# Kernel optimization log

Measured on AMD Instinct MI355X. Metric: run time of the kernel, lower is better.

Reference implementation:

```python
import jax, jax.numpy as jnp
import numpy as np

B, S, E, H, DK = 16, 512, 256, 8, 32
NSH, NSEL = 2, 4           # shared heads, selected dynamic heads
NDYN = H - NSH             # dynamic heads
NB = 4                     # num_blocks -> blocks_1: NB layers, blocks_2: 2*NB layers
L = 3 * NB                 # total layers, params stacked on leading dim
NSKILL, NQ = 1000, 10000
FC1, FC2 = 512, 256


def setup_inputs():
    key = jax.random.key(0)
    ks = jax.random.split(key, 24)
    r = lambda i, sh: jax.random.normal(ks[i], sh, jnp.float32) * 0.02
    return {
        'skills': jax.random.randint(ks[0], (B, S), 0, NSKILL),
        'responses': jax.random.randint(ks[1], (B, S), 0, 2),
        'questions': jax.random.randint(ks[2], (B, S), 0, NQ),
        'attention_mask': jnp.ones((B, S), jnp.int32),
        'q_embed': r(3, (NSKILL, E)),
        'qa_embed': r(4, (3, E)),
        'q_embed_diff': r(5, (NSKILL + 1, E)),
        'qa_embed_diff': r(6, (2 * NSKILL + 1, E)),
        'difficult_param': r(7, (NQ + 1, 1)),
        'Wq': r(8, (L, E, E)), 'bq': jnp.zeros((L, E)),
        'Wv': r(9, (L, E, E)), 'bv': jnp.zeros((L, E)),
        'Wo': r(10, (L, E, E)), 'bo': jnp.zeros((L, E)),
        'Wg': r(11, (L, E, NDYN)),
        'ln1_g': jnp.ones((L, E)), 'ln1_b': jnp.zeros((L, E)),
        'ln2_g': jnp.ones((L, E)), 'ln2_b': jnp.zeros((L, E)),
        'ffn_W1': r(12, (L, E, E)), 'ffn_b1': jnp.zeros((L, E)),
        'ffn_W2': r(13, (L, E, E)), 'ffn_b2': jnp.zeros((L, E)),
        'out_W1': r(14, (2 * E, FC1)), 'out_b1': jnp.zeros((FC1,)),
        'out_W2': r(15, (FC1, FC2)), 'out_b2': jnp.zeros((FC2,)),
        'out_W3': r(16, (FC2, 1)), 'out_b3': jnp.zeros((1,)),
    }


def _ln(x, g, b):
    m = x.mean(-1, keepdims=True)
    v = ((x - m) ** 2).mean(-1, keepdims=True)
    return (x - m) * jax.lax.rsqrt(v + 1e-5) * g + b


def _layer(i, q_in, k_in, v_in, mask, P):
    # MoH attention: standard MHA + top-k routed dynamic heads (kq_same=True)
    qh = (q_in @ P['Wq'][i] + P['bq'][i]).reshape(B, S, H, DK).transpose(0, 2, 1, 3)
    kh = (k_in @ P['Wq'][i] + P['bq'][i]).reshape(B, S, H, DK).transpose(0, 2, 1, 3)
    vh = (v_in @ P['Wv'][i] + P['bv'][i]).reshape(B, S, H, DK).transpose(0, 2, 1, 3)
    scores = jnp.einsum('bhid,bhjd->bhij', qh, kh) / np.float32(np.sqrt(DK))
    attn = jax.nn.softmax(jnp.where(mask, scores, -1e32), axis=-1)
    ctx = jnp.einsum('bhij,bhjd->bhid', attn, vh).transpose(0, 2, 1, 3)  # [B,S,H,DK]
    # router on pre-projection query: hard top-NSEL one-hot gates over NDYN heads
    logits = q_in @ P['Wg'][i]                     # [B,S,NDYN]
    _, topi = jax.lax.top_k(logits, NSEL)
    gates = jax.nn.one_hot(topi, NDYN, dtype=ctx.dtype).sum(-2)
    hg = jnp.concatenate([jnp.ones((B, S, NSH), ctx.dtype), gates], axis=-1)  # [B,S,H]
    attn_out = (ctx * hg[..., None]).reshape(B, S, E) @ P['Wo'][i] + P['bo'][i]
    x = _ln(q_in + attn_out, P['ln1_g'][i], P['ln1_b'][i])
    f = jax.nn.relu(x @ P['ffn_W1'][i] + P['ffn_b1'][i]) @ P['ffn_W2'][i] + P['ffn_b2'][i]
    return _ln(x + f, P['ln2_g'][i], P['ln2_b'][i])


def _forward(skills, responses, questions, P):
    masked_r = responses * (responses > -1).astype(responses.dtype)
    q_emb = P['q_embed'][skills]
    qa_emb = q_emb + P['qa_embed'][masked_r]
    q_diff = P['q_embed_diff'][skills]
    pid = P['difficult_param'][questions]          # [B,S,1]
    q_emb = q_emb + pid * q_diff
    qa_diff = P['qa_embed_diff'][skills + NSKILL * masked_r]
    qa_emb = qa_emb + pid * (qa_diff + q_diff)
    idx = jnp.arange(S)
    causal = (idx[None, :] <= idx[:, None])[None, None]  # mask==1: incl diagonal
    strict = (idx[None, :] < idx[:, None])[None, None]   # mask==0: excl diagonal
    y, x = qa_emb, q_emb
    for i in range(NB):
        y = _layer(i, y, y, y, causal, P)
    li = NB
    for _ in range(NB):
        x = _layer(li, x, x, x, causal, P); li += 1
        x = _layer(li, x, x, y, strict, P); li += 1
    h = jnp.concatenate([x, q_emb], axis=-1)
    h = jax.nn.relu(h @ P['out_W1'] + P['out_b1'])
    h = jax.nn.relu(h @ P['out_W2'] + P['out_b2'])
    out = jax.nn.sigmoid(h @ P['out_W3'] + P['out_b3'])[..., 0]
    return out[:, 1:]


def reference(skills, responses, questions, attention_mask, q_embed, qa_embed, q_embed_diff, qa_embed_diff, difficult_param, Wq, bq, Wv, bv, Wo, bo, Wg, ln1_g, ln1_b, ln2_g, ln2_b, ffn_W1, ffn_b1, ffn_W2, ffn_b2, out_W1, out_b1, out_W2, out_b2, out_W3, out_b3):
    P = dict(q_embed=q_embed, qa_embed=qa_embed, q_embed_diff=q_embed_diff, qa_embed_diff=qa_embed_diff, difficult_param=difficult_param, Wq=Wq, bq=bq, Wv=Wv, bv=bv, Wo=Wo, bo=bo, Wg=Wg, ln1_g=ln1_g, ln1_b=ln1_b, ln2_g=ln2_g, ln2_b=ln2_b, ffn_W1=ffn_W1, ffn_b1=ffn_b1, ffn_W2=ffn_W2, ffn_b2=ffn_b2, out_W1=out_W1, out_b1=out_b1, out_W2=out_W2, out_b2=out_b2, out_W3=out_W3, out_b3=out_b3)
    return _forward(skills, responses, questions, P)
```

## Files before the change

kernel.cpp:

```cpp
#include <hip/hip_runtime.h>
#include <hip/hip_bf16.h>

constexpr int CB = 16, CS = 512, CE = 256, CH = 8, CDK = 32;
constexpr int CNDYN = 6;
constexpr int CT = CB * CS;
constexpr float SCALE = 0.17677669529663687f;

typedef __bf16 bf16x8 __attribute__((ext_vector_type(8)));
typedef float f32x4 __attribute__((ext_vector_type(4)));
typedef unsigned short u16x8 __attribute__((ext_vector_type(8)));

__device__ __forceinline__ unsigned short f2bf(float x) {
    union { float f; unsigned u; } v; v.f = x;
    unsigned r = v.u + 0x7fff + ((v.u >> 16) & 1);
    return (unsigned short)(r >> 16);
}

__global__ __launch_bounds__(256) void embed_kernel(
    const int* __restrict__ skills, const int* __restrict__ responses,
    const int* __restrict__ questions,
    const float* __restrict__ q_embed, const float* __restrict__ qa_embed,
    const float* __restrict__ q_embed_diff, const float* __restrict__ qa_embed_diff,
    const float* __restrict__ difficult,
    float* __restrict__ q_emb, float* __restrict__ qa_emb, float* __restrict__ xb)
{
    int t = blockIdx.x;
    int e = threadIdx.x;
    int sk = skills[t];
    int r  = responses[t];
    r = (r > -1) ? r : 0;
    float pid = difficult[questions[t]];
    float qe  = q_embed[(size_t)sk * CE + e];
    float qd  = q_embed_diff[(size_t)sk * CE + e];
    float qv  = qe + pid * qd;
    float qae = qe + qa_embed[(size_t)r * CE + e];
    float qad = qa_embed_diff[((size_t)sk + 1000 * r) * CE + e];
    float qav = qae + pid * (qad + qd);
    q_emb[(size_t)t * CE + e]  = qv;
    xb[(size_t)t * CE + e]     = qv;
    qa_emb[(size_t)t * CE + e] = qav;
}

__device__ __forceinline__ void transpose_tile(
    const float* __restrict__ src, unsigned short* __restrict__ dst, int K, int N)
{
    __shared__ unsigned short T[64][72];
    int k0 = blockIdx.y * 64, n0 = blockIdx.x * 64;
    int t = threadIdx.x;
    int kr = t >> 3, nsg = (t & 7) * 8;
#pragma unroll
    for (int rr = 0; rr < 64; rr += 32) {
        const float* p = src + (size_t)(k0 + kr + rr) * N + n0 + nsg;
        float4 a = *reinterpret_cast<const float4*>(p);
        float4 b = *reinterpret_cast<const float4*>(p + 4);
        int k = kr + rr;
        T[nsg + 0][k] = f2bf(a.x); T[nsg + 1][k] = f2bf(a.y);
        T[nsg + 2][k] = f2bf(a.z); T[nsg + 3][k] = f2bf(a.w);
        T[nsg + 4][k] = f2bf(b.x); T[nsg + 5][k] = f2bf(b.y);
        T[nsg + 6][k] = f2bf(b.z); T[nsg + 7][k] = f2bf(b.w);
    }
    __syncthreads();
    {
        int n = t >> 2, ks = (t & 3) * 16;
        unsigned short* dp = dst + (size_t)(n0 + n) * K + k0 + ks;
        *reinterpret_cast<u16x8*>(dp)     = *reinterpret_cast<const u16x8*>(&T[n][ks]);
        *reinterpret_cast<u16x8*>(dp + 8) = *reinterpret_cast<const u16x8*>(&T[n][ks + 8]);
    }
}

__global__ __launch_bounds__(256) void prep_w_layers(
    const float* __restrict__ Wq, const float* __restrict__ Wv,
    const float* __restrict__ Wo, const float* __restrict__ W1,
    const float* __restrict__ W2,
    unsigned short* __restrict__ qvT, unsigned short* __restrict__ woT,
    unsigned short* __restrict__ w1T, unsigned short* __restrict__ w2T)
{
    int z = blockIdx.z;
    int which = z / 12, l = z % 12;
    const float* src;
    unsigned short* dst;
    if      (which == 0) { src = Wq + (size_t)l * 65536; dst = qvT + (size_t)l * 131072; }
    else if (which == 1) { src = Wv + (size_t)l * 65536; dst = qvT + (size_t)l * 131072 + 65536; }
    else if (which == 2) { src = Wo + (size_t)l * 65536; dst = woT + (size_t)l * 65536; }
    else if (which == 3) { src = W1 + (size_t)l * 65536; dst = w1T + (size_t)l * 65536; }
    else                 { src = W2 + (size_t)l * 65536; dst = w2T + (size_t)l * 65536; }
    transpose_tile(src, dst, 256, 256);
}

__global__ __launch_bounds__(256) void prep_w_one(
    const float* __restrict__ src, unsigned short* __restrict__ dst, int K, int N)
{
    transpose_tile(src, dst, K, N);
}

__global__ __launch_bounds__(256) void gemm_mfma(
    const float* __restrict__ A, const unsigned short* __restrict__ WT,
    const float* __restrict__ bias, float* __restrict__ C,
    const float* __restrict__ bias2, float* __restrict__ C2,
    const unsigned char* __restrict__ gmask,
    int M, int N, int K, int relu, int split)
{
    __shared__ __attribute__((aligned(16))) unsigned short As[64][72];
    __shared__ __attribute__((aligned(16))) unsigned short Bs[64][72];
    int tid = threadIdx.x;
    int bm = blockIdx.y * 64, bn = blockIdx.x * 64;
    int w = tid >> 6, lane = tid & 63;
    int wr = w >> 1, wc = w & 1;
    int lo = lane & 15, hi = lane >> 4;
    int srow = tid >> 2, sseg = (tid & 3) * 16;
    f32x4 acc[2][2] = {};

    for (int kk = 0; kk < K; kk += 64) {
        {
            const float* ap = A + (size_t)(bm + srow) * K + kk + sseg;
            float4 a0 = *reinterpret_cast<const float4*>(ap);
            float4 a1 = *reinterpret_cast<const float4*>(ap + 4);
            float4 a2 = *reinterpret_cast<const float4*>(ap + 8);
            float4 a3 = *reinterpret_cast<const float4*>(ap + 12);
            if (gmask) {
                int hh = (kk + sseg) >> 5;
                float km = ((gmask[bm + srow] >> hh) & 1) ? 1.f : 0.f;
                a0.x*=km; a0.y*=km; a0.z*=km; a0.w*=km;
                a1.x*=km; a1.y*=km; a1.z*=km; a1.w*=km;
                a2.x*=km; a2.y*=km; a2.z*=km; a2.w*=km;
                a3.x*=km; a3.y*=km; a3.z*=km; a3.w*=km;
            }
            u16x8 p0, p1;
            p0[0]=f2bf(a0.x); p0[1]=f2bf(a0.y); p0[2]=f2bf(a0.z); p0[3]=f2bf(a0.w);
            p0[4]=f2bf(a1.x); p0[5]=f2bf(a1.y); p0[6]=f2bf(a1.z); p0[7]=f2bf(a1.w);
            p1[0]=f2bf(a2.x); p1[1]=f2bf(a2.y); p1[2]=f2bf(a2.z); p1[3]=f2bf(a2.w);
            p1[4]=f2bf(a3.x); p1[5]=f2bf(a3.y); p1[6]=f2bf(a3.z); p1[7]=f2bf(a3.w);
            *reinterpret_cast<u16x8*>(&As[srow][sseg])     = p0;
            *reinterpret_cast<u16x8*>(&As[srow][sseg + 8]) = p1;
            const unsigned short* bp = WT + (size_t)(bn + srow) * K + kk + sseg;
            *reinterpret_cast<u16x8*>(&Bs[srow][sseg])     = *reinterpret_cast<const u16x8*>(bp);
            *reinterpret_cast<u16x8*>(&Bs[srow][sseg + 8]) = *reinterpret_cast<const u16x8*>(bp + 8);
        }
        __syncthreads();
#pragma unroll
        for (int ks = 0; ks < 2; ++ks) {
            bf16x8 a0 = *reinterpret_cast<const bf16x8*>(&As[wr * 32 + lo][ks * 32 + hi * 8]);
            bf16x8 a1 = *reinterpret_cast<const bf16x8*>(&As[wr * 32 + 16 + lo][ks * 32 + hi * 8]);
            bf16x8 b0 = *reinterpret_cast<const bf16x8*>(&Bs[wc * 32 + lo][ks * 32 + hi * 8]);
            bf16x8 b1 = *reinterpret_cast<const bf16x8*>(&Bs[wc * 32 + 16 + lo][ks * 32 + hi * 8]);
            acc[0][0] = __builtin_amdgcn_mfma_f32_16x16x32_bf16(a0, b0, acc[0][0], 0, 0, 0);
            acc[0][1] = __builtin_amdgcn_mfma_f32_16x16x32_bf16(a0, b1, acc[0][1], 0, 0, 0);
            acc[1][0] = __builtin_amdgcn_mfma_f32_16x16x32_bf16(a1, b0, acc[1][0], 0, 0, 0);
            acc[1][1] = __builtin_amdgcn_mfma_f32_16x16x32_bf16(a1, b1, acc[1][1], 0, 0, 0);
        }
        __syncthreads();
    }
    const float* bp = bias;
    float* Cp = C;
    int ldc = split ? split : N;
    int cb = bn;
    if (split && bn >= split) { bp = bias2; Cp = C2; ldc = N - split; cb = bn - split; }
#pragma unroll
    for (int i = 0; i < 2; ++i)
#pragma unroll
        for (int j = 0; j < 2; ++j) {
            int col = cb + wc * 32 + j * 16 + lo;
            float bv = bp[col];
#pragma unroll
            for (int r = 0; r < 4; ++r) {
                int row = bm + wr * 32 + i * 16 + hi * 4 + r;
                float v = acc[i][j][r] + bv;
                if (relu) v = fmaxf(v, 0.f);
                Cp[(size_t)row * ldc + col] = v;
            }
        }
}

__global__ __launch_bounds__(256) void attn_mfma(
    const float* __restrict__ Q, const float* __restrict__ V,
    float* __restrict__ Ctx, int strict)
{
    __shared__ __attribute__((aligned(16))) unsigned short Qs[64][40];
    __shared__ __attribute__((aligned(16))) unsigned short Ks[64][40];
    __shared__ __attribute__((aligned(16))) unsigned short VTs[32][72];
    __shared__ __attribute__((aligned(16))) unsigned short Ps[4][16][72];

    int blk = blockIdx.x;
    int qt = blk & 7;
    int h  = (blk >> 3) & 7;
    int b  = blk >> 6;
    int tid = threadIdx.x;
    int w = tid >> 6, lane = tid & 63;
    int lo = lane & 15, hi = lane >> 4;
    int qbase = qt * 64;
    int qg = qbase + w * 16 + lo;
    bool uni = strict && (qg == 0);

    {
        int row = tid >> 2, d0 = (tid & 3) * 8;
        const float* p = Q + ((size_t)b * CS + qbase + row) * CE + h * 32 + d0;
        float4 a = *reinterpret_cast<const float4*>(p);
        float4 c = *reinterpret_cast<const float4*>(p + 4);
        unsigned short* dst = &Qs[row][d0];
        dst[0]=f2bf(a.x); dst[1]=f2bf(a.y); dst[2]=f2bf(a.z); dst[3]=f2bf(a.w);
        dst[4]=f2bf(c.x); dst[5]=f2bf(c.y); dst[6]=f2bf(c.z); dst[7]=f2bf(c.w);
    }
    __syncthreads();
    bf16x8 qfrag = *reinterpret_cast<const bf16x8*>(&Qs[w * 16 + lo][hi * 8]);

    f32x4 ctx0 = {0.f,0.f,0.f,0.f}, ctx1 = {0.f,0.f,0.f,0.f};
    float m = -1e30f, l = 0.f;

    int ntiles = (strict && qt == 0) ? (CS / 64) : (qt + 1);
    for (int t = 0; t < ntiles; ++t) {
        int k64 = t * 64;
        {
            int row = tid >> 2, d0 = (tid & 3) * 8;
            const float* kp = Q + ((size_t)b * CS + k64 + row) * CE + h * 32 + d0;
            float4 a = *reinterpret_cast<const float4*>(kp);
            float4 c = *reinterpret_cast<const float4*>(kp + 4);
            unsigned short* dst = &Ks[row][d0];
            dst[0]=f2bf(a.x); dst[1]=f2bf(a.y); dst[2]=f2bf(a.z); dst[3]=f2bf(a.w);
            dst[4]=f2bf(c.x); dst[5]=f2bf(c.y); dst[6]=f2bf(c.z); dst[7]=f2bf(c.w);
            const float* vp = V + ((size_t)b * CS + k64 + row) * CE + h * 32 + d0;
            float4 va = *reinterpret_cast<const float4*>(vp);
            float4 vc = *reinterpret_cast<const float4*>(vp + 4);
            VTs[d0+0][row]=f2bf(va.x); VTs[d0+1][row]=f2bf(va.y);
            VTs[d0+2][row]=f2bf(va.z); VTs[d0+3][row]=f2bf(va.w);
            VTs[d0+4][row]=f2bf(vc.x); VTs[d0+5][row]=f2bf(vc.y);
            VTs[d0+6][row]=f2bf(vc.z); VTs[d0+7][row]=f2bf(vc.w);
        }
        __syncthreads();

        f32x4 sacc[4];
#pragma unroll
        for (int kt = 0; kt < 4; ++kt) {
            bf16x8 kfrag = *reinterpret_cast<const bf16x8*>(&Ks[kt * 16 + lo][hi * 8]);
            f32x4 z = {0.f,0.f,0.f,0.f};
            sacc[kt] = __builtin_amdgcn_mfma_f32_16x16x32_bf16(kfrag, qfrag, z, 0, 0, 0);
        }
        float sv[16];
        float mt = -1e30f;
#pragma unroll
        for (int kt = 0; kt < 4; ++kt)
#pragma unroll
            for (int r = 0; r < 4; ++r) {
                int kidx = k64 + kt * 16 + hi * 4 + r;
                float s = sacc[kt][r] * SCALE;
                bool valid = strict ? (kidx < qg) : (kidx <= qg);
                s = valid ? s : -1e30f;
                if (uni) s = 0.f;
                sv[kt * 4 + r] = s;
                mt = fmaxf(mt, s);
            }
        mt = fmaxf(mt, __shfl_xor(mt, 16));
        mt = fmaxf(mt, __shfl_xor(mt, 32));
        float mn = fmaxf(m, mt);
        float co = __expf(m - mn);
        float lt = 0.f;
#pragma unroll
        for (int i = 0; i < 16; ++i) {
            float p = __expf(sv[i] - mn);
            sv[i] = p;
            lt += p;
        }
        lt += __shfl_xor(lt, 16);
        lt += __shfl_xor(lt, 32);
        l = l * co + lt;
        m = mn;
#pragma unroll
        for (int r = 0; r < 4; ++r) { ctx0[r] *= co; ctx1[r] *= co; }
#pragma unroll
        for (int kt = 0; kt < 4; ++kt) {
            unsigned short* pd = &Ps[w][lo][kt * 16 + hi * 4];
            pd[0] = f2bf(sv[kt * 4 + 0]); pd[1] = f2bf(sv[kt * 4 + 1]);
            pd[2] = f2bf(sv[kt * 4 + 2]); pd[3] = f2bf(sv[kt * 4 + 3]);
        }
        __syncthreads();
#pragma unroll
        for (int kh = 0; kh < 2; ++kh) {
            bf16x8 pfrag = *reinterpret_cast<const bf16x8*>(&Ps[w][lo][kh * 32 + hi * 8]);
            bf16x8 v0 = *reinterpret_cast<const bf16x8*>(&VTs[lo][kh * 32 + hi * 8]);
            bf16x8 v1 = *reinterpret_cast<const bf16x8*>(&VTs[16 + lo][kh * 32 + hi * 8]);
            ctx0 = __builtin_amdgcn_mfma_f32_16x16x32_bf16(v0, pfrag, ctx0, 0, 0, 0);
            ctx1 = __builtin_amdgcn_mfma_f32_16x16x32_bf16(v1, pfrag, ctx1, 0, 0, 0);
        }
        __syncthreads();
    }

    float inv = 1.f / l;
    float* cb = reinterpret_cast<float*>(&Ps[w][0][0]);
#pragma unroll
    for (int r = 0; r < 4; ++r) {
        cb[lo * 36 + (hi * 4 + r)]      = ctx0[r] * inv;
        cb[lo * 36 + (16 + hi * 4 + r)] = ctx1[r] * inv;
    }
    __syncthreads();
    {
        int qloc = lane >> 2, d0 = (lane & 3) * 8;
        const float* src = cb + qloc * 36 + d0;
        float4 o0 = *reinterpret_cast<const float4*>(src);
        float4 o1 = *reinterpret_cast<const float4*>(src + 4);
        int i = qbase + w * 16 + qloc;
        float* op = Ctx + ((size_t)b * CS + i) * CE + h * 32 + d0;
        *reinterpret_cast<float4*>(op)     = o0;
        *reinterpret_cast<float4*>(op + 4) = o1;
    }
}

__global__ __launch_bounds__(64) void gate_mask(
    const float* __restrict__ qin, const float* __restrict__ Wg,
    unsigned char* __restrict__ mb)
{
    int t = blockIdx.x;
    int lane = threadIdx.x;
    const float* q = qin + (size_t)t * CE;
    float p[CNDYN] = {};
#pragma unroll
    for (int r = 0; r < 4; ++r) {
        int e = lane + r * 64;
        float qe = q[e];
        const float* wg = &Wg[(size_t)e * CNDYN];
#pragma unroll
        for (int j = 0; j < CNDYN; ++j) p[j] += qe * wg[j];
    }
#pragma unroll
    for (int o = 32; o > 0; o >>= 1)
#pragma unroll
        for (int j = 0; j < CNDYN; ++j) p[j] += __shfl_down(p[j], o);
    if (lane == 0) {
        int mask = 3;
        for (int j = 0; j < CNDYN; ++j) {
            int rank = 0;
            for (int k = 0; k < CNDYN; ++k)
                if (p[k] > p[j] || (p[k] == p[j] && k < j)) rank++;
            if (rank < 4) mask |= 1 << (2 + j);
        }
        mb[t] = (unsigned char)mask;
    }
}

__global__ __launch_bounds__(256) void add_ln(
    const float* __restrict__ A, const float* __restrict__ Bv,
    const float* __restrict__ g, const float* __restrict__ bb,
    float* __restrict__ O)
{
    int w = threadIdx.x >> 6, lane = threadIdx.x & 63;
    int t = blockIdx.x * 4 + w;
    size_t base = (size_t)t * CE + lane * 4;
    float4 a = *reinterpret_cast<const float4*>(A + base);
    float4 b = *reinterpret_cast<const float4*>(Bv + base);
    float4 v = {a.x + b.x, a.y + b.y, a.z + b.z, a.w + b.w};
    float s = v.x + v.y + v.z + v.w;
#pragma unroll
    for (int o = 32; o > 0; o >>= 1) s += __shfl_xor(s, o);
    float mean = s * (1.f / CE);
    float4 d = {v.x - mean, v.y - mean, v.z - mean, v.w - mean};
    float s2 = d.x * d.x + d.y * d.y + d.z * d.z + d.w * d.w;
#pragma unroll
    for (int o = 32; o > 0; o >>= 1) s2 += __shfl_xor(s2, o);
    float rstd = rsqrtf(s2 * (1.f / CE) + 1e-5f);
    float4 gg = *reinterpret_cast<const float4*>(g + lane * 4);
    float4 bv4 = *reinterpret_cast<const float4*>(bb + lane * 4);
    float4 o4 = {d.x * rstd * gg.x + bv4.x, d.y * rstd * gg.y + bv4.y,
                 d.z * rstd * gg.z + bv4.z, d.w * rstd * gg.w + bv4.w};
    *reinterpret_cast<float4*>(O + base) = o4;
}

__global__ __launch_bounds__(256) void concat_kernel(
    const float* __restrict__ x, const float* __restrict__ qe,
    float* __restrict__ cat)
{
    int t = blockIdx.x, e = threadIdx.x;
    cat[(size_t)t * 512 + e]       = x[(size_t)t * CE + e];
    cat[(size_t)t * 512 + 256 + e] = qe[(size_t)t * CE + e];
}

__global__ __launch_bounds__(64) void final_kernel(
    const float* __restrict__ H2, const float* __restrict__ W3,
    const float* __restrict__ b3, float* __restrict__ out)
{
    int t = blockIdx.x, lane = threadIdx.x;
    const float* h = H2 + (size_t)t * CE;
    float s = 0.f;
#pragma unroll
    for (int r = 0; r < 4; ++r) {
        int e = lane + r * 64;
        s += h[e] * W3[e];
    }
#pragma unroll
    for (int o = 32; o > 0; o >>= 1) s += __shfl_down(s, o);
    if (lane == 0) {
        float v = 1.f / (1.f + __expf(-(s + b3[0])));
        int b = t >> 9, si = t & 511;
        if (si > 0) out[(size_t)b * (CS - 1) + si - 1] = v;
    }
}

extern "C" void kernel_launch(void* const* d_in, const int* in_sizes, int n_in,
                              void* d_out, int out_size, void* d_ws, size_t ws_size,
                              hipStream_t stream)
{
    const int* skills    = (const int*)d_in[0];
    const int* responses = (const int*)d_in[1];
    const int* questions = (const int*)d_in[2];
    const float* q_embed       = (const float*)d_in[4];
    const float* qa_embed      = (const float*)d_in[5];
    const float* q_embed_diff  = (const float*)d_in[6];
    const float* qa_embed_diff = (const float*)d_in[7];
    const float* difficult     = (const float*)d_in[8];
    const float* Wq = (const float*)d_in[9];  const float* bq = (const float*)d_in[10];
    const float* Wv = (const float*)d_in[11]; const float* bv = (const float*)d_in[12];
    const float* Wo = (const float*)d_in[13]; const float* bo = (const float*)d_in[14];
    const float* Wg = (const float*)d_in[15];
    const float* ln1g = (const float*)d_in[16]; const float* ln1b = (const float*)d_in[17];
    const float* ln2g = (const float*)d_in[18]; const float* ln2b = (const float*)d_in[19];
    const float* fW1 = (const float*)d_in[20]; const float* fb1 = (const float*)d_in[21];
    const float* fW2 = (const float*)d_in[22]; const float* fb2 = (const float*)d_in[23];
    const float* oW1 = (const float*)d_in[24]; const float* ob1 = (const float*)d_in[25];
    const float* oW2 = (const float*)d_in[26]; const float* ob2 = (const float*)d_in[27];
    const float* oW3 = (const float*)d_in[28]; const float* ob3 = (const float*)d_in[29];
    float* out = (float*)d_out;

    char* ws = (char*)d_ws;
    const size_t R = (size_t)CT * CE * sizeof(float);
    float* q_emb = (float*)(ws + 0 * R);
    float* xb    = (float*)(ws + 1 * R);
    float* yb    = (float*)(ws + 2 * R);
    float* S0    = (float*)(ws + 3 * R);
    float* S1    = (float*)(ws + 4 * R);
    float* S2    = (float*)(ws + 5 * R);
    unsigned short* qvT = (unsigned short*)(ws + 7 * R);
    unsigned short* woT = qvT + (size_t)12 * 131072;
    unsigned short* w1T = woT + (size_t)12 * 65536;
    unsigned short* w2T = w1T + (size_t)12 * 65536;
    unsigned short* o1T = w2T + (size_t)12 * 65536;
    unsigned short* o2T = o1T + (size_t)512 * 512;
    unsigned char* maskbuf = (unsigned char*)(o2T + (size_t)256 * 512);
    (void)in_sizes; (void)n_in; (void)out_size; (void)ws_size;

    prep_w_layers<<<dim3(4, 4, 60), 256, 0, stream>>>(Wq, Wv, Wo, fW1, fW2, qvT, woT, w1T, w2T);
    prep_w_one<<<dim3(8, 8), 256, 0, stream>>>(oW1, o1T, 512, 512);
    prep_w_one<<<dim3(4, 8), 256, 0, stream>>>(oW2, o2T, 512, 256);

    embed_kernel<<<CT, 256, 0, stream>>>(skills, responses, questions,
        q_embed, qa_embed, q_embed_diff, qa_embed_diff, difficult, q_emb, yb, xb);

    auto layer = [&](int li, const float* qin, const float* vin, float* outc, int strict) {
        if (qin == vin) {
            gemm_mfma<<<dim3(8, 128), 256, 0, stream>>>(qin, qvT + (size_t)li * 131072,
                bq + (size_t)li * CE, S0, bv + (size_t)li * CE, S1, nullptr,
                CT, 512, CE, 0, 256);
        } else {
            gemm_mfma<<<dim3(4, 128), 256, 0, stream>>>(qin, qvT + (size_t)li * 131072,
                bq + (size_t)li * CE, S0, nullptr, nullptr, nullptr, CT, CE, CE, 0, 0);
            gemm_mfma<<<dim3(4, 128), 256, 0, stream>>>(vin, qvT + (size_t)li * 131072 + 65536,
                bv + (size_t)li * CE, S1, nullptr, nullptr, nullptr, CT, CE, CE, 0, 0);
        }
        gate_mask<<<CT, 64, 0, stream>>>(qin, Wg + (size_t)li * CE * CNDYN, maskbuf);
        attn_mfma<<<CB * CH * 8, 256, 0, stream>>>(S0, S1, S2, strict);
        gemm_mfma<<<dim3(4, 128), 256, 0, stream>>>(S2, woT + (size_t)li * 65536,
            bo + (size_t)li * CE, S0, nullptr, nullptr, maskbuf, CT, CE, CE, 0, 0);
        add_ln<<<CT / 4, 256, 0, stream>>>(qin, S0, ln1g + (size_t)li * CE, ln1b + (size_t)li * CE, S1);
        gemm_mfma<<<dim3(4, 128), 256, 0, stream>>>(S1, w1T + (size_t)li * 65536,
            fb1 + (size_t)li * CE, S2, nullptr, nullptr, nullptr, CT, CE, CE, 1, 0);
        gemm_mfma<<<dim3(4, 128), 256, 0, stream>>>(S2, w2T + (size_t)li * 65536,
            fb2 + (size_t)li * CE, S0, nullptr, nullptr, nullptr, CT, CE, CE, 0, 0);
        add_ln<<<CT / 4, 256, 0, stream>>>(S1, S0, ln2g + (size_t)li * CE, ln2b + (size_t)li * CE, outc);
    };

    for (int i = 0; i < 4; ++i) layer(i, yb, yb, yb, 0);
    int li = 4;
    for (int r = 0; r < 4; ++r) {
        layer(li, xb, xb, xb, 0); li++;
        layer(li, xb, yb, xb, 1); li++;
    }

    concat_kernel<<<CT, 256, 0, stream>>>(xb, q_emb, S0);
    gemm_mfma<<<dim3(8, 128), 256, 0, stream>>>(S0, o1T, ob1, S2, nullptr, nullptr, nullptr, CT, 512, 512, 1, 0);
    gemm_mfma<<<dim3(4, 128), 256, 0, stream>>>(S2, o2T, ob2, xb, nullptr, nullptr, nullptr, CT, 256, 512, 1, 0);
    final_kernel<<<CT, 64, 0, stream>>>(xb, oW3, ob3, out);
}
```

Before: 1.242 ms.

## Stage full per-head K/V in LDS and process all query groups per block

The attention kernel now loads the whole 512-row K and transposed V for one (batch, head) into shared memory once. 512-thread blocks loop over query groups, and each block covers half of the sequence. Within a wave, block-wide barriers are replaced by LDS waitcnt plus sched_barrier, since each wave uses its own P buffer. This removes the repeated K/V global loads and bf16 conversions across query tiles, along with the per-tile __syncthreads. The cost is roughly 96KB of LDS per block, fewer blocks, and uneven causal work between the two halves. gate_mask is also regrouped to handle 8 tokens per 512-thread block, cutting the launch count.

After: 1.161 ms. 1.07x faster.

```diff
diff --git a/kernel.cpp b/kernel.cpp
--- a/kernel.cpp
+++ b/kernel.cpp
@@ -171,144 +171,141 @@
         }
 }
 
-__global__ __launch_bounds__(256) void attn_mfma(
+__global__ __launch_bounds__(512) void attn_mfma(
     const float* __restrict__ Q, const float* __restrict__ V,
     float* __restrict__ Ctx, int strict)
 {
-    __shared__ __attribute__((aligned(16))) unsigned short Qs[64][40];
-    __shared__ __attribute__((aligned(16))) unsigned short Ks[64][40];
-    __shared__ __attribute__((aligned(16))) unsigned short VTs[32][72];
-    __shared__ __attribute__((aligned(16))) unsigned short Ps[4][16][72];
+    __shared__ __attribute__((aligned(16))) unsigned short Ks[512][40];
+    __shared__ __attribute__((aligned(16))) unsigned short VTc[8][32][72];
+    __shared__ __attribute__((aligned(16))) unsigned short Ps[8][16][72];
 
     int blk = blockIdx.x;
-    int qt = blk & 7;
-    int h  = (blk >> 3) & 7;
-    int b  = blk >> 6;
+    int half = blk & 1;
+    int h = (blk >> 1) & 7;
+    int b = blk >> 4;
     int tid = threadIdx.x;
     int w = tid >> 6, lane = tid & 63;
     int lo = lane & 15, hi = lane >> 4;
-    int qbase = qt * 64;
-    int qg = qbase + w * 16 + lo;
-    bool uni = strict && (qg == 0);
-
-    {
-        int row = tid >> 2, d0 = (tid & 3) * 8;
-        const float* p = Q + ((size_t)b * CS + qbase + row) * CE + h * 32 + d0;
-        float4 a = *reinterpret_cast<const float4*>(p);
-        float4 c = *reinterpret_cast<const float4*>(p + 4);
-        unsigned short* dst = &Qs[row][d0];
+
+#pragma unroll
+    for (int r = 0; r < 4; ++r) {
+        int row = (tid >> 2) + r * 128;
+        int d0 = (tid & 3) * 8;
+        const float* kp = Q + ((size_t)b * CS + row) * CE + h * 32 + d0;
+        float4 a = *reinterpret_cast<const float4*>(kp);
+        float4 c = *reinterpret_cast<const float4*>(kp + 4);
+        unsigned short* dst = &Ks[row][d0];
         dst[0]=f2bf(a.x); dst[1]=f2bf(a.y); dst[2]=f2bf(a.z); dst[3]=f2bf(a.w);
         dst[4]=f2bf(c.x); dst[5]=f2bf(c.y); dst[6]=f2bf(c.z); dst[7]=f2bf(c.w);
+        const float* vp = V + ((size_t)b * CS + row) * CE + h * 32 + d0;
+        float4 va = *reinterpret_cast<const float4*>(vp);
+        float4 vc = *reinterpret_cast<const float4*>(vp + 4);
+        int c8 = row >> 6, kc = row & 63;
+        VTc[c8][d0+0][kc]=f2bf(va.x); VTc[c8][d0+1][kc]=f2bf(va.y);
+        VTc[c8][d0+2][kc]=f2bf(va.z); VTc[c8][d0+3][kc]=f2bf(va.w);
+        VTc[c8][d0+4][kc]=f2bf(vc.x); VTc[c8][d0+5][kc]=f2bf(vc.y);
+        VTc[c8][d0+6][kc]=f2bf(vc.z); VTc[c8][d0+7][kc]=f2bf(vc.w);
     }
     __syncthreads();
-    bf16x8 qfrag = *reinterpret_cast<const bf16x8*>(&Qs[w * 16 + lo][hi * 8]);
-
-    f32x4 ctx0 = {0.f,0.f,0.f,0.f}, ctx1 = {0.f,0.f,0.f,0.f};
-    float m = -1e30f, l = 0.f;
-
-    int ntiles = (strict && qt == 0) ? (CS / 64) : (qt + 1);
-    for (int t = 0; t < ntiles; ++t) {
-        int k64 = t * 64;
+
+    for (int it = 0; it < 2; ++it) {
+        int gg = half * 16 + w + it * 8;
+        int qg0 = gg * 16;
+        int qg = qg0 + lo;
+        bool uni = strict && (qg == 0);
+        bf16x8 qfrag = *reinterpret_cast<const bf16x8*>(&Ks[qg0 + lo][hi * 8]);
+
+        f32x4 ctx0 = {0.f,0.f,0.f,0.f}, ctx1 = {0.f,0.f,0.f,0.f};
+        float m = -1e30f, l = 0.f;
+        int nch = (strict && qg0 == 0) ? 8 : ((gg >> 2) + 1);
+
+        for (int c = 0; c < nch; ++c) {
+            f32x4 sacc[4];
+#pragma unroll
+            for (int kt = 0; kt < 4; ++kt) {
+                bf16x8 kfrag = *reinterpret_cast<const bf16x8*>(&Ks[c * 64 + kt * 16 + lo][hi * 8]);
+                f32x4 z = {0.f,0.f,0.f,0.f};
+                sacc[kt] = __builtin_amdgcn_mfma_f32_16x16x32_bf16(kfrag, qfrag, z, 0, 0, 0);
+            }
+            float sv[16];
+            float mt = -1e30f;
+#pragma unroll
+            for (int kt = 0; kt < 4; ++kt)
+#pragma unroll
+                for (int r = 0; r < 4; ++r) {
+                    int kidx = c * 64 + kt * 16 + hi * 4 + r;
+                    float s = sacc[kt][r] * SCALE;
+                    bool valid = strict ? (kidx < qg) : (kidx <= qg);
+                    s = valid ? s : -1e30f;
+                    if (uni) s = 0.f;
+                    sv[kt * 4 + r] = s;
+                    mt = fmaxf(mt, s);
+                }
+            mt = fmaxf(mt, __shfl_xor(mt, 16));
+            mt = fmaxf(mt, __shfl_xor(mt, 32));
+            float mn = fmaxf(m, mt);
+            float co = __expf(m - mn);
+            float lt = 0.f;
+#pragma unroll
+            for (int i = 0; i < 16; ++i) {
+                float p = __expf(sv[i] - mn);
+                sv[i] = p;
+                lt += p;
+            }
+            lt += __shfl_xor(lt, 16);
+            lt += __shfl_xor(lt, 32);
+            l = l * co + lt;
+            m = mn;
+#pragma unroll
+            for (int r = 0; r < 4; ++r) { ctx0[r] *= co; ctx1[r] *= co; }
+#pragma unroll
+            for (int kt = 0; kt < 4; ++kt) {
+                unsigned short* pd = &Ps[w][lo][kt * 16 + hi * 4];
+                pd[0] = f2bf(sv[kt * 4 + 0]); pd[1] = f2bf(sv[kt * 4 + 1]);
+                pd[2] = f2bf(sv[kt * 4 + 2]); pd[3] = f2bf(sv[kt * 4 + 3]);
+            }
+            asm volatile("s_waitcnt lgkmcnt(0)" ::: "memory");
+            __builtin_amdgcn_sched_barrier(0);
+#pragma unroll
+            for (int kh = 0; kh < 2; ++kh) {
+                bf16x8 pfrag = *reinterpret_cast<const bf16x8*>(&Ps[w][lo][kh * 32 + hi * 8]);
+                bf16x8 v0 = *reinterpret_cast<const bf16x8*>(&VTc[c][lo][kh * 32 + hi * 8]);
+                bf16x8 v1 = *reinterpret_cast<const bf16x8*>(&VTc[c][16 + lo][kh * 32 + hi * 8]);
+                ctx0 = __builtin_amdgcn_mfma_f32_16x16x32_bf16(v0, pfrag, ctx0, 0, 0, 0);
+                ctx1 = __builtin_amdgcn_mfma_f32_16x16x32_bf16(v1, pfrag, ctx1, 0, 0, 0);
+            }
+        }
+
+        float inv = 1.f / l;
+        float* cb = reinterpret_cast<float*>(&Ps[w][0][0]);
+#pragma unroll
+        for (int r = 0; r < 4; ++r) {
+            cb[lo * 36 + (hi * 4 + r)]      = ctx0[r] * inv;
+            cb[lo * 36 + (16 + hi * 4 + r)] = ctx1[r] * inv;
+        }
+        asm volatile("s_waitcnt lgkmcnt(0)" ::: "memory");
+        __builtin_amdgcn_sched_barrier(0);
         {
-            int row = tid >> 2, d0 = (tid & 3) * 8;
-            const float* kp = Q + ((size_t)b * CS + k64 + row) * CE + h * 32 + d0;
-            float4 a = *reinterpret_cast<const float4*>(kp);
-            float4 c = *reinterpret_cast<const float4*>(kp + 4);
-            unsigned short* dst = &Ks[row][d0];
-            dst[0]=f2bf(a.x); dst[1]=f2bf(a.y); dst[2]=f2bf(a.z); dst[3]=f2bf(a.w);
-            dst[4]=f2bf(c.x); dst[5]=f2bf(c.y); dst[6]=f2bf(c.z); dst[7]=f2bf(c.w);
-            const float* vp = V + ((size_t)b * CS + k64 + row) * CE + h * 32 + d0;
-            float4 va = *reinterpret_cast<const float4*>(vp);
-            float4 vc = *reinterpret_cast<const float4*>(vp + 4);
-            VTs[d0+0][row]=f2bf(va.x); VTs[d0+1][row]=f2bf(va.y);
-            VTs[d0+2][row]=f2bf(va.z); VTs[d0+3][row]=f2bf(va.w);
-            VTs[d0+4][row]=f2bf(vc.x); VTs[d0+5][row]=f2bf(vc.y);
-            VTs[d0+6][row]=f2bf(vc.z); VTs[d0+7][row]=f2bf(vc.w);
-        }
-        __syncthreads();
-
-        f32x4 sacc[4];
-#pragma unroll
-        for (int kt = 0; kt < 4; ++kt) {
-            bf16x8 kfrag = *reinterpret_cast<const bf16x8*>(&Ks[kt * 16 + lo][hi * 8]);
-            f32x4 z = {0.f,0.f,0.f,0.f};
-            sacc[kt] = __builtin_amdgcn_mfma_f32_16x16x32_bf16(kfrag, qfrag, z, 0, 0, 0);
-        }
-        float sv[16];
-        float mt = -1e30f;
-#pragma unroll
-        for (int kt = 0; kt < 4; ++kt)
-#pragma unroll
-            for (int r = 0; r < 4; ++r) {
-                int kidx = k64 + kt * 16 + hi * 4 + r;
-                float s = sacc[kt][r] * SCALE;
-                bool valid = strict ? (kidx < qg) : (kidx <= qg);
-                s = valid ? s : -1e30f;
-                if (uni) s = 0.f;
-                sv[kt * 4 + r] = s;
-                mt = fmaxf(mt, s);
-            }
-        mt = fmaxf(mt, __shfl_xor(mt, 16));
-        mt = fmaxf(mt, __shfl_xor(mt, 32));
-        float mn = fmaxf(m, mt);
-        float co = __expf(m - mn);
-        float lt = 0.f;
-#pragma unroll
-        for (int i = 0; i < 16; ++i) {
-            float p = __expf(sv[i] - mn);
-            sv[i] = p;
-            lt += p;
-        }
-        lt += __shfl_xor(lt, 16);
-        lt += __shfl_xor(lt, 32);
-        l = l * co + lt;
-        m = mn;
-#pragma unroll
-        for (int r = 0; r < 4; ++r) { ctx0[r] *= co; ctx1[r] *= co; }
-#pragma unroll
-        for (int kt = 0; kt < 4; ++kt) {
-            unsigned short* pd = &Ps[w][lo][kt * 16 + hi * 4];
-            pd[0] = f2bf(sv[kt * 4 + 0]); pd[1] = f2bf(sv[kt * 4 + 1]);
-            pd[2] = f2bf(sv[kt * 4 + 2]); pd[3] = f2bf(sv[kt * 4 + 3]);
-        }
-        __syncthreads();
-#pragma unroll
-        for (int kh = 0; kh < 2; ++kh) {
-            bf16x8 pfrag = *reinterpret_cast<const bf16x8*>(&Ps[w][lo][kh * 32 + hi * 8]);
-            bf16x8 v0 = *reinterpret_cast<const bf16x8*>(&VTs[lo][kh * 32 + hi * 8]);
-            bf16x8 v1 = *reinterpret_cast<const bf16x8*>(&VTs[16 + lo][kh * 32 + hi * 8]);
-            ctx0 = __builtin_amdgcn_mfma_f32_16x16x32_bf16(v0, pfrag, ctx0, 0, 0, 0);
-            ctx1 = __builtin_amdgcn_mfma_f32_16x16x32_bf16(v1, pfrag, ctx1, 0, 0, 0);
-        }
-        __syncthreads();
-    }
-
-    float inv = 1.f / l;
-    float* cb = reinterpret_cast<float*>(&Ps[w][0][0]);
-#pragma unroll
-    for (int r = 0; r < 4; ++r) {
-        cb[lo * 36 + (hi * 4 + r)]      = ctx0[r] * inv;
-        cb[lo * 36 + (16 + hi * 4 + r)] = ctx1[r] * inv;
-    }
-    __syncthreads();
-    {
-        int qloc = lane >> 2, d0 = (lane & 3) * 8;
-        const float* src = cb + qloc * 36 + d0;
-        float4 o0 = *reinterpret_cast<const float4*>(src);
-        float4 o1 = *reinterpret_cast<const float4*>(src + 4);
-        int i = qbase + w * 16 + qloc;
-        float* op = Ctx + ((size_t)b * CS + i) * CE + h * 32 + d0;
-        *reinterpret_cast<float4*>(op)     = o0;
-        *reinterpret_cast<float4*>(op + 4) = o1;
-    }
-}
-
-__global__ __launch_bounds__(64) void gate_mask(
+            int qloc = lane >> 2, d0 = (lane & 3) * 8;
+            const float* src = cb + qloc * 36 + d0;
+            float4 o0 = *reinterpret_cast<const float4*>(src);
+            float4 o1 = *reinterpret_cast<const float4*>(src + 4);
+            int i = qg0 + qloc;
+            float* op = Ctx + ((size_t)b * CS + i) * CE + h * 32 + d0;
+            *reinterpret_cast<float4*>(op)     = o0;
+            *reinterpret_cast<float4*>(op + 4) = o1;
+        }
+        asm volatile("s_waitcnt lgkmcnt(0)" ::: "memory");
+        __builtin_amdgcn_sched_barrier(0);
+    }
+}
+
+__global__ __launch_bounds__(512) void gate_mask(
     const float* __restrict__ qin, const float* __restrict__ Wg,
     unsigned char* __restrict__ mb)
 {
-    int t = blockIdx.x;
-    int lane = threadIdx.x;
+    int w = threadIdx.x >> 6, lane = threadIdx.x & 63;
+    int t = blockIdx.x * 8 + w;
     const float* q = qin + (size_t)t * CE;
     float p[CNDYN] = {};
 #pragma unroll
@@ -452,8 +449,8 @@
             gemm_mfma<<<dim3(4, 128), 256, 0, stream>>>(vin, qvT + (size_t)li * 131072 + 65536,
                 bv + (size_t)li * CE, S1, nullptr, nullptr, nullptr, CT, CE, CE, 0, 0);
         }
-        gate_mask<<<CT, 64, 0, stream>>>(qin, Wg + (size_t)li * CE * CNDYN, maskbuf);
-        attn_mfma<<<CB * CH * 8, 256, 0, stream>>>(S0, S1, S2, strict);
+        gate_mask<<<CT / 8, 512, 0, stream>>>(qin, Wg + (size_t)li * CE * CNDYN, maskbuf);
+        attn_mfma<<<CB * CH * 2, 512, 0, stream>>>(S0, S1, S2, strict);
         gemm_mfma<<<dim3(4, 128), 256, 0, stream>>>(S2, woT + (size_t)li * 65536,
             bo + (size_t)li * CE, S0, nullptr, nullptr, maskbuf, CT, CE, CE, 0, 0);
         add_ln<<<CT / 4, 256, 0, stream>>>(qin, S0, ln1g + (size_t)li * CE, ln1b + (size_t)li * CE, S1);
```
